# Kernel optimization log

Measured on AMD Instinct MI355X. Metric: run time of the kernel, lower is better.

The kernel has to match this reference:

```python
import jax, jax.numpy as jnp
import numpy as np

RC = 6.0  # cosine cutoff radius (cut_fn)
ZETAS = np.array([1.0, 2.0, 4.0, 16.0], dtype=np.float32)


def _cut(r):
    # Behler cosine cutoff: 0.5*(cos(pi*r/rc)+1) for r<rc else 0
    return jnp.where(r < RC, 0.5 * (jnp.cos(jnp.pi * r / RC) + 1.0), 0.0)


def setup_inputs() -> dict:
    key = jax.random.key(0)
    k1, k2, k3, k4, k5 = jax.random.split(key, 5)
    B, N, T, E = 8, 512, 512, 8
    r_ij = jax.random.uniform(k1, (B, N, T), dtype=jnp.float32) * 5.0 + 0.5
    r_ik = jax.random.uniform(k2, (B, N, T), dtype=jnp.float32) * 5.0 + 0.5
    theta = jax.random.uniform(k3, (B, N, T), dtype=jnp.float32) * np.pi
    # law of cosines -> valid triangle, so cos_theta in [-1, 1]
    r_jk = jnp.sqrt(r_ij ** 2 + r_ik ** 2 - 2.0 * r_ij * r_ik * jnp.cos(theta))
    mask_triples = jax.random.randint(k4, (B, N, T), 0, 2).astype(jnp.int32)
    etas = jax.random.uniform(k5, (E,), dtype=jnp.float32) + 0.5
    return {"r_ij": r_ij, "r_ik": r_ik, "r_jk": r_jk,
            "mask_triples": mask_triples, "etas": etas}


def reference(r_ij, r_ik, r_jk, mask_triples, etas):
    zetas = jnp.asarray(ZETAS, dtype=r_ij.dtype)          # [Z]
    valid = (mask_triples != 0)                            # [B,N,T]
    valid4 = valid[..., None]                              # broadcast over feature dim

    # radial part: exp(-eta*(r_ij^2+r_ik^2)) * fc(r_ij)*fc(r_ik)   [B,N,T,E]
    r2 = r_ij ** 2 + r_ik ** 2
    radius = jnp.exp(-etas * r2[..., None]) * (_cut(r_ij) * _cut(r_ik))[..., None]
    radius = jnp.where(valid4, radius, 0.0)

    # angular part (faithful to source: both branches use (1 - cos)^zeta)
    cos_t = (r2 - r_jk ** 2) / (2.0 * r_ij * r_ik)
    cos_t = jnp.where(valid, cos_t, 0.0)
    base = (1.0 - cos_t)[..., None] ** zetas               # [B,N,T,Z]
    ang = jnp.concatenate([2.0 ** (1.0 - zetas) * base,
                           2.0 ** (1.0 + zetas) * base], axis=-1)  # [B,N,T,2Z]
    ang = jnp.where(valid4, ang, 0.0)

    # fused outer-product + reduce over triples (avoids [B,N,T,E,2Z] tensor)
    f = jnp.einsum('bnte,bnta->bnea', radius, ang)         # [B,N,E,2Z]
    B, N = r_ij.shape[:2]
    return f.reshape(B, N, -1)
```

## Files before the change

kernel.cpp:

```cpp
#include <hip/hip_runtime.h>

#define LOG2E 1.4426950408889634f

template<int M, int HALF>
__device__ __forceinline__ void rs_round(float* v, int lane) {
  const bool up = (lane & M) != 0;
#pragma unroll
  for (int i = 0; i < HALF; ++i) {
    float send = up ? v[i] : v[i + HALF];
    float recv = __shfl_xor(send, M, 64);
    v[i] = (up ? v[i + HALF] : v[i]) + recv;
  }
}

__global__ __launch_bounds__(256, 4) void behler_g3_kernel(
    const float* __restrict__ r_ij, const float* __restrict__ r_ik,
    const float* __restrict__ r_jk, const int* __restrict__ mask,
    const float* __restrict__ etas, float* __restrict__ out)
{
  const int tid  = threadIdx.x;
  const int lane = tid & 63;
  const int wave = tid >> 6;
  const int row  = blockIdx.x * 4 + wave;

  float c[8];
#pragma unroll
  for (int e = 0; e < 8; ++e) c[e] = -etas[e] * LOG2E;

  float v[32];
#pragma unroll
  for (int i = 0; i < 32; ++i) v[i] = 0.0f;

  const size_t base = (size_t)row * 512;
  const float4* pij = (const float4*)(r_ij + base);
  const float4* pik = (const float4*)(r_ik + base);
  const float4* pjk = (const float4*)(r_jk + base);
  const int4*   pm  = (const int4*)(mask + base);

#pragma unroll
  for (int k = 0; k < 2; ++k) {
    const int idx = k * 64 + lane;
    const float4 vij = pij[idx];
    const float4 vik = pik[idx];
    const float4 vjk = pjk[idx];
    const int4   vm  = pm[idx];
#pragma unroll
    for (int u = 0; u < 4; ++u) {
      const float rij = (u == 0) ? vij.x : (u == 1) ? vij.y : (u == 2) ? vij.z : vij.w;
      const float rik = (u == 0) ? vik.x : (u == 1) ? vik.y : (u == 2) ? vik.z : vik.w;
      const float rjk = (u == 0) ? vjk.x : (u == 1) ? vjk.y : (u == 2) ? vjk.z : vjk.w;
      const int   m   = (u == 0) ? vm.x  : (u == 1) ? vm.y  : (u == 2) ? vm.z  : vm.w;

      const float r2  = fmaf(rik, rik, rij * rij);
      const float num = fmaf(-rjk, rjk, r2);
      const float ct  = (0.5f * num) * __builtin_amdgcn_rcpf(rij * rik);
      const float x   = 1.0f - ct;
      const float fci = __builtin_amdgcn_cosf(rij * (1.0f / 12.0f)) + 1.0f;
      const float fck = __builtin_amdgcn_cosf(rik * (1.0f / 12.0f)) + 1.0f;
      float fcp = 0.25f * fci * fck;
      fcp = (m != 0) ? fcp : 0.0f;

      const float x2 = x * x, x4 = x2 * x2, x8 = x4 * x4, x16 = x8 * x8;
      const float b0 = x * fcp, b1 = x2 * fcp, b2 = x4 * fcp, b3 = x16 * fcp;

#pragma unroll
      for (int e = 0; e < 8; ++e) {
        const float w = __builtin_amdgcn_exp2f(c[e] * r2);
        v[e * 4 + 0] = fmaf(w, b0, v[e * 4 + 0]);
        v[e * 4 + 1] = fmaf(w, b1, v[e * 4 + 1]);
        v[e * 4 + 2] = fmaf(w, b2, v[e * 4 + 2]);
        v[e * 4 + 3] = fmaf(w, b3, v[e * 4 + 3]);
      }
    }
  }

  rs_round<1, 16>(v, lane);
  rs_round<2, 8>(v, lane);
  rs_round<4, 4>(v, lane);
  rs_round<8, 2>(v, lane);
  rs_round<16, 1>(v, lane);
  v[0] += __shfl_xor(v[0], 32, 64);

  const int vidx = __brev(lane & 31) >> 27;
  const int e = vidx >> 2;
  const int z = vidx & 3;

  float coef;
  int aoff;
  if (lane < 32) {
    coef = (z == 0) ? 1.0f : (z == 1) ? 0.5f : (z == 2) ? 0.125f : 3.0517578125e-05f;
    aoff = z;
  } else {
    coef = (z == 0) ? 4.0f : (z == 1) ? 8.0f : (z == 2) ? 32.0f : 131072.0f;
    aoff = 4 + z;
  }
  out[(size_t)row * 64 + e * 8 + aoff] = v[0] * coef;
}

extern "C" void kernel_launch(void* const* d_in, const int* in_sizes, int n_in,
                              void* d_out, int out_size, void* d_ws, size_t ws_size,
                              hipStream_t stream) {
  const float* r_ij = (const float*)d_in[0];
  const float* r_ik = (const float*)d_in[1];
  const float* r_jk = (const float*)d_in[2];
  const int*   mask = (const int*)d_in[3];
  const float* etas = (const float*)d_in[4];
  float* out = (float*)d_out;

  const int rows   = in_sizes[0] / 512;
  const int blocks = rows / 4;

  behler_g3_kernel<<<blocks, 256, 0, stream>>>(r_ij, r_ik, r_jk, mask, etas, out);
}
```

Baseline: 13.14 us.

## Split each row across two waves and combine partial sums through LDS

```diff
diff --git a/kernel.cpp b/kernel.cpp
--- a/kernel.cpp
+++ b/kernel.cpp
@@ -1,6 +1,6 @@
 #include <hip/hip_runtime.h>
 
-#define LOG2E 1.4426950408889634f
+#define NLOG2E -1.4426950408889634f
 
 template<int M, int HALF>
 __device__ __forceinline__ void rs_round(float* v, int lane) {
@@ -13,7 +13,7 @@
   }
 }
 
-__global__ __launch_bounds__(256, 4) void behler_g3_kernel(
+__global__ __launch_bounds__(256, 6) void behler_g3_kernel(
     const float* __restrict__ r_ij, const float* __restrict__ r_ik,
     const float* __restrict__ r_jk, const int* __restrict__ mask,
     const float* __restrict__ etas, float* __restrict__ out)
@@ -21,56 +21,47 @@
   const int tid  = threadIdx.x;
   const int lane = tid & 63;
   const int wave = tid >> 6;
-  const int row  = blockIdx.x * 4 + wave;
+  const int half = wave & 1;
+  const int row  = blockIdx.x * 2 + (wave >> 1);
 
-  float c[8];
-#pragma unroll
-  for (int e = 0; e < 8; ++e) c[e] = -etas[e] * LOG2E;
+  const size_t base = (size_t)row * 512 + (size_t)half * 256;
+  const float4 vij = ((const float4*)(r_ij + base))[lane];
+  const float4 vik = ((const float4*)(r_ik + base))[lane];
+  const float4 vjk = ((const float4*)(r_jk + base))[lane];
+  const int4   vm  = ((const int4*)(mask + base))[lane];
+  const float* fij = (const float*)&vij;
+  const float* fik = (const float*)&vik;
+  const float* fjk = (const float*)&vjk;
+  const int*   im  = (const int*)&vm;
 
   float v[32];
 #pragma unroll
   for (int i = 0; i < 32; ++i) v[i] = 0.0f;
 
-  const size_t base = (size_t)row * 512;
-  const float4* pij = (const float4*)(r_ij + base);
-  const float4* pik = (const float4*)(r_ik + base);
-  const float4* pjk = (const float4*)(r_jk + base);
-  const int4*   pm  = (const int4*)(mask + base);
+#pragma unroll
+  for (int u = 0; u < 4; ++u) {
+    const float rij = fij[u], rik = fik[u], rjk = fjk[u];
 
+    const float r2  = fmaf(rik, rik, rij * rij);
+    const float num = fmaf(-rjk, rjk, r2);
+    const float ct  = (0.5f * num) * __builtin_amdgcn_rcpf(rij * rik);
+    const float x   = 1.0f - ct;
+    const float fci = __builtin_amdgcn_cosf(rij * (1.0f / 12.0f)) + 1.0f;
+    const float fck = __builtin_amdgcn_cosf(rik * (1.0f / 12.0f)) + 1.0f;
+    float fcp = fci * fck;
+    fcp = (im[u] != 0) ? fcp : 0.0f;
+
+    const float x2 = x * x, x4 = x2 * x2, x8 = x4 * x4, x16 = x8 * x8;
+    const float b0 = x * fcp, b1 = x2 * fcp, b2 = x4 * fcp, b3 = x16 * fcp;
+
+    const float r2n = r2 * NLOG2E;
 #pragma unroll
-  for (int k = 0; k < 2; ++k) {
-    const int idx = k * 64 + lane;
-    const float4 vij = pij[idx];
-    const float4 vik = pik[idx];
-    const float4 vjk = pjk[idx];
-    const int4   vm  = pm[idx];
-#pragma unroll
-    for (int u = 0; u < 4; ++u) {
-      const float rij = (u == 0) ? vij.x : (u == 1) ? vij.y : (u == 2) ? vij.z : vij.w;
-      const float rik = (u == 0) ? vik.x : (u == 1) ? vik.y : (u == 2) ? vik.z : vik.w;
-      const float rjk = (u == 0) ? vjk.x : (u == 1) ? vjk.y : (u == 2) ? vjk.z : vjk.w;
-      const int   m   = (u == 0) ? vm.x  : (u == 1) ? vm.y  : (u == 2) ? vm.z  : vm.w;
-
-      const float r2  = fmaf(rik, rik, rij * rij);
-      const float num = fmaf(-rjk, rjk, r2);
-      const float ct  = (0.5f * num) * __builtin_amdgcn_rcpf(rij * rik);
-      const float x   = 1.0f - ct;
-      const float fci = __builtin_amdgcn_cosf(rij * (1.0f / 12.0f)) + 1.0f;
-      const float fck = __builtin_amdgcn_cosf(rik * (1.0f / 12.0f)) + 1.0f;
-      float fcp = 0.25f * fci * fck;
-      fcp = (m != 0) ? fcp : 0.0f;
-
-      const float x2 = x * x, x4 = x2 * x2, x8 = x4 * x4, x16 = x8 * x8;
-      const float b0 = x * fcp, b1 = x2 * fcp, b2 = x4 * fcp, b3 = x16 * fcp;
-
-#pragma unroll
-      for (int e = 0; e < 8; ++e) {
-        const float w = __builtin_amdgcn_exp2f(c[e] * r2);
-        v[e * 4 + 0] = fmaf(w, b0, v[e * 4 + 0]);
-        v[e * 4 + 1] = fmaf(w, b1, v[e * 4 + 1]);
-        v[e * 4 + 2] = fmaf(w, b2, v[e * 4 + 2]);
-        v[e * 4 + 3] = fmaf(w, b3, v[e * 4 + 3]);
-      }
+    for (int e = 0; e < 8; ++e) {
+      const float w = __builtin_amdgcn_exp2f(r2n * etas[e]);
+      v[e * 4 + 0] = fmaf(w, b0, v[e * 4 + 0]);
+      v[e * 4 + 1] = fmaf(w, b1, v[e * 4 + 1]);
+      v[e * 4 + 2] = fmaf(w, b2, v[e * 4 + 2]);
+      v[e * 4 + 3] = fmaf(w, b3, v[e * 4 + 3]);
     }
   }
 
@@ -81,20 +72,28 @@
   rs_round<16, 1>(v, lane);
   v[0] += __shfl_xor(v[0], 32, 64);
 
+  __shared__ float lds[4][64];
+  lds[wave][lane] = v[0];
+  __syncthreads();
+  const float sum = v[0] + lds[wave ^ 1][lane];
+
   const int vidx = __brev(lane & 31) >> 27;
   const int e = vidx >> 2;
   const int z = vidx & 3;
 
-  float coef;
-  int aoff;
-  if (lane < 32) {
-    coef = (z == 0) ? 1.0f : (z == 1) ? 0.5f : (z == 2) ? 0.125f : 3.0517578125e-05f;
-    aoff = z;
-  } else {
-    coef = (z == 0) ? 4.0f : (z == 1) ? 8.0f : (z == 2) ? 32.0f : 131072.0f;
-    aoff = 4 + z;
+  if ((lane >> 5) == half) {
+    float coef;
+    int aoff;
+    if (half == 0) {
+      coef = (z == 0) ? 0.25f : (z == 1) ? 0.125f : (z == 2) ? 0.03125f
+                                                             : 7.62939453125e-06f;
+      aoff = z;
+    } else {
+      coef = (z == 0) ? 1.0f : (z == 1) ? 2.0f : (z == 2) ? 8.0f : 32768.0f;
+      aoff = 4 + z;
+    }
+    out[(size_t)row * 64 + e * 8 + aoff] = sum * coef;
   }
-  out[(size_t)row * 64 + e * 8 + aoff] = v[0] * coef;
 }
 
 extern "C" void kernel_launch(void* const* d_in, const int* in_sizes, int n_in,
@@ -108,7 +107,7 @@
   float* out = (float*)d_out;
 
   const int rows   = in_sizes[0] / 512;
-  const int blocks = rows / 4;
+  const int blocks = rows / 2;
 
   behler_g3_kernel<<<blocks, 256, 0, stream>>>(r_ij, r_ik, r_jk, mask, etas, out);
 }
```

New measurement: 13.23 us. About the same (+0.7%).
